# Kernel tuning notes

Measured on AMD Instinct MI355X. Metric: run time of the kernel, lower is better.

The kernel has to match this reference:

```python
import jax, jax.numpy as jnp
import numpy as np

N, K, R = 32768, 4096, 256

def setup_inputs() -> dict:
    key = jax.random.key(0)
    k1, k2, k3 = jax.random.split(key, 3)
    H = jax.random.normal(k1, (N, R), dtype=jnp.float32)
    L = jax.random.normal(k2, (K, R), dtype=jnp.float32)
    W_I = jax.random.normal(k3, (R, R), dtype=jnp.float32)
    return {"H": H, "L": L, "W_I": W_I}

def reference(H, L, W_I):
    # Q = W_I @ L^T : (r, k)
    Q = jnp.einsum('rs,ks->rk', W_I, L)
    # M_I = H @ Q : (n, k)
    M_I = jnp.einsum('nr,rk->nk', H, Q)
    A_I = jax.nn.softmax(M_I, axis=1)
    # C_I = A_I @ L : (n, r)
    C_I = jnp.einsum('nk,kr->nr', A_I, L)
    return (C_I, A_I)
```

## Files before the change

### kernel.cpp

```cpp
#include <hip/hip_runtime.h>
#include <hip/hip_bf16.h>
#include <math.h>
#include <stdint.h>

constexpr int N_ROWS = 32768;
constexpr int K_DIM  = 4096;
constexpr int R_DIM  = 256;
constexpr int KP     = 3 * R_DIM;
constexpr int KB     = K_DIM / 128;

typedef __bf16 bf16x8 __attribute__((ext_vector_type(8)));
typedef float  f32x4  __attribute__((ext_vector_type(4)));
typedef unsigned short u16x8 __attribute__((ext_vector_type(8)));
typedef unsigned short u16x4 __attribute__((ext_vector_type(4)));

__device__ __forceinline__ unsigned short f2bf(float x) {
    unsigned u = __float_as_uint(x);
    u += 0x7fffu + ((u >> 16) & 1u);
    return (unsigned short)(u >> 16);
}
__device__ __forceinline__ float bf2f(unsigned short h) {
    return __uint_as_float((unsigned)h << 16);
}

__device__ __forceinline__ void gl2lds16(const void* gptr, void* lptr) {
    __builtin_amdgcn_global_load_lds(
        (const __attribute__((address_space(1))) unsigned int*)gptr,
        (__attribute__((address_space(3))) unsigned int*)lptr,
        16, 0, 0);
}

__global__ __launch_bounds__(256)
void gemm_mfma_nt(const unsigned short* __restrict__ A,
                  const unsigned short* __restrict__ B,
                  float* __restrict__ C,
                  float* __restrict__ Pm, float* __restrict__ Ps,
                  int M, int N, int Kc)
{
    __shared__ __align__(16) unsigned short As[128 * 32];
    __shared__ __align__(16) unsigned short Bs[128 * 32];
    __shared__ float pm_s[128][2], ps_s[128][2];

    const int tid  = threadIdx.x;
    const int wave = tid >> 6, lane = tid & 63;
    const int wm = wave >> 1, wn = wave & 1;
    const long m0 = (long)blockIdx.x * 128;
    const long n0 = (long)blockIdx.y * 128;

    f32x4 acc[4][4] = {};

    const int srow  = lane >> 2;
    const int skoff = (lane & 3) * 8;
    const int c0 = wave, c1 = wave + 4;
    const int kq = (lane >> 4) * 8;
    const int mr = lane & 15;

    for (int k0 = 0; k0 < Kc; k0 += 32) {
        gl2lds16(A + (m0 + c0 * 16 + srow) * (long)Kc + k0 + skoff, &As[c0 * 512]);
        gl2lds16(A + (m0 + c1 * 16 + srow) * (long)Kc + k0 + skoff, &As[c1 * 512]);
        gl2lds16(B + (n0 + c0 * 16 + srow) * (long)Kc + k0 + skoff, &Bs[c0 * 512]);
        gl2lds16(B + (n0 + c1 * 16 + srow) * (long)Kc + k0 + skoff, &Bs[c1 * 512]);
        __syncthreads();

        bf16x8 af[4], bfr[4];
#pragma unroll
        for (int t = 0; t < 4; ++t) {
            af[t]  = *(const bf16x8*)&As[(wm * 64 + t * 16 + mr) * 32 + kq];
            bfr[t] = *(const bf16x8*)&Bs[(wn * 64 + t * 16 + mr) * 32 + kq];
        }
#pragma unroll
        for (int i = 0; i < 4; ++i)
#pragma unroll
            for (int j = 0; j < 4; ++j)
                acc[i][j] = __builtin_amdgcn_mfma_f32_16x16x32_bf16(
                    af[i], bfr[j], acc[i][j], 0, 0, 0);
        __syncthreads();
    }

    const int col = lane & 15, rquad = (lane >> 4) * 4;
#pragma unroll
    for (int i = 0; i < 4; ++i) {
        const long mrow = m0 + wm * 64 + i * 16 + rquad;
#pragma unroll
        for (int j = 0; j < 4; ++j) {
            float* p = C + mrow * (long)N + n0 + wn * 64 + j * 16 + col;
#pragma unroll
            for (int r = 0; r < 4; ++r) p[(long)r * N] = acc[i][j][r];
        }
    }

#pragma unroll
    for (int i = 0; i < 4; ++i) {
#pragma unroll
        for (int r = 0; r < 4; ++r) {
            float mx = fmaxf(fmaxf(acc[i][0][r], acc[i][1][r]),
                             fmaxf(acc[i][2][r], acc[i][3][r]));
#pragma unroll
            for (int off = 1; off < 16; off <<= 1)
                mx = fmaxf(mx, __shfl_xor(mx, off));
            float sm = 0.f;
#pragma unroll
            for (int j = 0; j < 4; ++j) sm += __expf(acc[i][j][r] - mx);
#pragma unroll
            for (int off = 1; off < 16; off <<= 1)
                sm += __shfl_xor(sm, off);
            if (mr == 0) {
                const int rw = wm * 64 + i * 16 + rquad + r;
                pm_s[rw][wn] = mx;
                ps_s[rw][wn] = sm;
            }
        }
    }
    __syncthreads();
    if (tid < 128) {
        const float ma = pm_s[tid][0], mb = pm_s[tid][1];
        const float mx = fmaxf(ma, mb);
        const float s  = ps_s[tid][0] * __expf(ma - mx) +
                         ps_s[tid][1] * __expf(mb - mx);
        Pm[(m0 + tid) * KB + blockIdx.y] = mx;
        Ps[(m0 + tid) * KB + blockIdx.y] = s;
    }
}

__global__ __launch_bounds__(256)
void finalize_ms(const float* __restrict__ Pm, const float* __restrict__ Ps,
                 float* __restrict__ SMm, float* __restrict__ SMi)
{
    const long row = (long)blockIdx.x * 256 + threadIdx.x;
    const float4* pm = (const float4*)(Pm + row * KB);
    const float4* ps = (const float4*)(Ps + row * KB);
    float4 v[8];
    float mx = -3.4e38f;
#pragma unroll
    for (int q = 0; q < 8; ++q) {
        v[q] = pm[q];
        mx = fmaxf(mx, fmaxf(fmaxf(v[q].x, v[q].y), fmaxf(v[q].z, v[q].w)));
    }
    float s = 0.f;
#pragma unroll
    for (int q = 0; q < 8; ++q) {
        float4 w = ps[q];
        s += w.x * __expf(v[q].x - mx) + w.y * __expf(v[q].y - mx) +
             w.z * __expf(v[q].z - mx) + w.w * __expf(v[q].w - mx);
    }
    SMm[row] = mx;
    SMi[row] = 1.f / s;
}

__global__ __launch_bounds__(512)
void softmax_av_pv(float* __restrict__ Mio,
                   const unsigned short* __restrict__ LT,
                   const float* __restrict__ SMm, const float* __restrict__ SMi,
                   float* __restrict__ C)
{
    __shared__ __align__(16) unsigned short Bs[R_DIM * 64];
    __shared__ __align__(16) unsigned short As[64 * 64];
    __shared__ float sm_m[64], sm_inv[64];

    const int tid  = threadIdx.x;
    const int wave = tid >> 6, lane = tid & 63;
    const long m0 = (long)blockIdx.x * 64;

    if (tid < 64) { sm_m[tid] = SMm[m0 + tid]; sm_inv[tid] = SMi[m0 + tid]; }
    __syncthreads();

    f32x4 acc[2][4] = {};
    const int wm = wave >> 2, wn = wave & 3;
    const int mr = lane & 15;
    const int kq16 = (lane >> 4) * 16;

    for (int k0 = 0; k0 < K_DIM; k0 += 64) {
#pragma unroll
        for (int q = 0; q < 4; ++q) {
            const int rbase = q * 64 + wave * 8;
            const int rloc  = rbase + (lane >> 3);
            const int phys  = (lane & 7) * 16;
            const int kbyte = phys ^ ((rloc & 7) << 4);
            gl2lds16((const char*)LT + (long)rloc * (K_DIM * 2) + (long)k0 * 2 + kbyte,
                     &Bs[rbase * 64]);
        }
#pragma unroll
        for (int p = 0; p < 2; ++p) {
            const int row = p * 32 + wave * 4 + (lane >> 4);
            const int col = (lane & 15) * 4;
            float* gp = Mio + (m0 + row) * (long)K_DIM + k0 + col;
            float4 v = *(const float4*)gp;
            const float mrow = sm_m[row], inv = sm_inv[row];
            float e0 = __expf(v.x - mrow), e1 = __expf(v.y - mrow);
            float e2 = __expf(v.z - mrow), e3 = __expf(v.w - mrow);
            *(float4*)gp = make_float4(e0 * inv, e1 * inv, e2 * inv, e3 * inv);
            u16x4 u;
            u[0] = f2bf(e0); u[1] = f2bf(e1); u[2] = f2bf(e2); u[3] = f2bf(e3);
            const int byte = (row * 128 + col * 2) ^ ((row & 7) << 4);
            *(u16x4*)((char*)As + byte) = u;
        }
        __syncthreads();

#pragma unroll
        for (int ks = 0; ks < 2; ++ks) {
            bf16x8 af[2], bfr[4];
#pragma unroll
            for (int t = 0; t < 2; ++t) {
                const int arow = wm * 32 + t * 16 + mr;
                const int ab = (arow * 128 + ks * 64 + kq16) ^ ((arow & 7) << 4);
                af[t] = *(const bf16x8*)((const char*)As + ab);
            }
#pragma unroll
            for (int t = 0; t < 4; ++t) {
                const int brow = wn * 64 + t * 16 + mr;
                const int bb = (brow * 128 + ks * 64 + kq16) ^ ((brow & 7) << 4);
                bfr[t] = *(const bf16x8*)((const char*)Bs + bb);
            }
#pragma unroll
            for (int i = 0; i < 2; ++i)
#pragma unroll
                for (int j = 0; j < 4; ++j)
                    acc[i][j] = __builtin_amdgcn_mfma_f32_16x16x32_bf16(
                        af[i], bfr[j], acc[i][j], 0, 0, 0);
        }
        __syncthreads();
    }

    const int col = lane & 15, rquad = (lane >> 4) * 4;
#pragma unroll
    for (int i = 0; i < 2; ++i) {
        const int lrow0 = wm * 32 + i * 16 + rquad;
#pragma unroll
        for (int j = 0; j < 4; ++j) {
            float* p = C + (m0 + lrow0) * (long)R_DIM + wn * 64 + j * 16 + col;
#pragma unroll
            for (int r = 0; r < 4; ++r)
                p[(long)r * R_DIM] = acc[i][j][r] * sm_inv[lrow0 + r];
        }
    }
}

__global__ __launch_bounds__(256)
void prep_B(const float* __restrict__ L, unsigned short* __restrict__ Bp)
{
    const long i = (long)blockIdx.x * 256 + threadIdx.x;
    const long k = i >> 8; const int r = (int)(i & 255);
    const float x = L[i];
    const unsigned short hi = f2bf(x);
    const unsigned short lo = f2bf(x - bf2f(hi));
    unsigned short* row = Bp + k * KP;
    row[r] = hi; row[R_DIM + r] = lo; row[2 * R_DIM + r] = hi;
}

__global__ __launch_bounds__(256)
void prep_LT(const float* __restrict__ L, unsigned short* __restrict__ LT)
{
    const long i = (long)blockIdx.x * 256 + threadIdx.x;
    const long r = i >> 12; const long k = i & 4095;
    LT[r * K_DIM + k] = f2bf(L[k * R_DIM + r]);
}

template<bool BT>
__global__ __launch_bounds__(256)
void gemm128(const float* __restrict__ A, const float* __restrict__ B,
             float* __restrict__ C, int M, int N, int Kc)
{
    __shared__ __align__(16) float Asl[16][132];
    __shared__ __align__(16) float Bsl[16][132];

    const int tid = threadIdx.x;
    const int tx = tid & 15, ty = tid >> 4;
    const long m0 = (long)blockIdx.x * 128;
    const long n0 = (long)blockIdx.y * 128;

    float acc[8][8];
#pragma unroll
    for (int i = 0; i < 8; ++i)
#pragma unroll
        for (int j = 0; j < 8; ++j) acc[i][j] = 0.f;

    for (int k0 = 0; k0 < Kc; k0 += 16) {
#pragma unroll
        for (int q = 0; q < 2; ++q) {
            int fi = tid + 256 * q, row = fi >> 2, col = (fi & 3) * 4;
            float4 v = *(const float4*)(A + (m0 + row) * (long)Kc + k0 + col);
            Asl[col + 0][row] = v.x; Asl[col + 1][row] = v.y;
            Asl[col + 2][row] = v.z; Asl[col + 3][row] = v.w;
        }
        if (BT) {
#pragma unroll
            for (int q = 0; q < 2; ++q) {
                int fi = tid + 256 * q, row = fi >> 2, col = (fi & 3) * 4;
                float4 v = *(const float4*)(B + (n0 + row) * (long)Kc + k0 + col);
                Bsl[col + 0][row] = v.x; Bsl[col + 1][row] = v.y;
                Bsl[col + 2][row] = v.z; Bsl[col + 3][row] = v.w;
            }
        } else {
#pragma unroll
            for (int q = 0; q < 2; ++q) {
                int fi = tid + 256 * q, row = fi >> 5, col = (fi & 31) * 4;
                float4 v = *(const float4*)(B + (k0 + row) * (long)N + n0 + col);
                *(float4*)&Bsl[row][col] = v;
            }
        }
        __syncthreads();
#pragma unroll
        for (int kk = 0; kk < 16; ++kk) {
            float a[8], b[8];
            *(float4*)&a[0] = *(const float4*)&Asl[kk][ty * 8];
            *(float4*)&a[4] = *(const float4*)&Asl[kk][ty * 8 + 4];
            *(float4*)&b[0] = *(const float4*)&Bsl[kk][tx * 8];
            *(float4*)&b[4] = *(const float4*)&Bsl[kk][tx * 8 + 4];
#pragma unroll
            for (int i = 0; i < 8; ++i)
#pragma unroll
                for (int j = 0; j < 8; ++j)
                    acc[i][j] = fmaf(a[i], b[j], acc[i][j]);
        }
        __syncthreads();
    }
#pragma unroll
    for (int i = 0; i < 8; ++i) {
        float* p = C + (m0 + ty * 8 + i) * (long)N + n0 + tx * 8;
        *(float4*)p       = make_float4(acc[i][0], acc[i][1], acc[i][2], acc[i][3]);
        *(float4*)(p + 4) = make_float4(acc[i][4], acc[i][5], acc[i][6], acc[i][7]);
    }
}

__global__ __launch_bounds__(256)
void gemm128_hl(const float* __restrict__ A, const float* __restrict__ B,
                unsigned short* __restrict__ Ap, int M, int N, int Kc)
{
    __shared__ __align__(16) float Asl[16][132];
    __shared__ __align__(16) float Bsl[16][132];

    const int tid = threadIdx.x;
    const int tx = tid & 15, ty = tid >> 4;
    const long m0 = (long)blockIdx.x * 128;
    const long n0 = (long)blockIdx.y * 128;

    float acc[8][8];
#pragma unroll
    for (int i = 0; i < 8; ++i)
#pragma unroll
        for (int j = 0; j < 8; ++j) acc[i][j] = 0.f;

    for (int k0 = 0; k0 < Kc; k0 += 16) {
#pragma unroll
        for (int q = 0; q < 2; ++q) {
            int fi = tid + 256 * q, row = fi >> 2, col = (fi & 3) * 4;
            float4 v = *(const float4*)(A + (m0 + row) * (long)Kc + k0 + col);
            Asl[col + 0][row] = v.x; Asl[col + 1][row] = v.y;
            Asl[col + 2][row] = v.z; Asl[col + 3][row] = v.w;
        }
#pragma unroll
        for (int q = 0; q < 2; ++q) {
            int fi = tid + 256 * q, row = fi >> 5, col = (fi & 31) * 4;
            float4 v = *(const float4*)(B + (k0 + row) * (long)N + n0 + col);
            *(float4*)&Bsl[row][col] = v;
        }
        __syncthreads();
#pragma unroll
        for (int kk = 0; kk < 16; ++kk) {
            float a[8], b[8];
            *(float4*)&a[0] = *(const float4*)&Asl[kk][ty * 8];
            *(float4*)&a[4] = *(const float4*)&Asl[kk][ty * 8 + 4];
            *(float4*)&b[0] = *(const float4*)&Bsl[kk][tx * 8];
            *(float4*)&b[4] = *(const float4*)&Bsl[kk][tx * 8 + 4];
#pragma unroll
            for (int i = 0; i < 8; ++i)
#pragma unroll
                for (int j = 0; j < 8; ++j)
                    acc[i][j] = fmaf(a[i], b[j], acc[i][j]);
        }
        __syncthreads();
    }
#pragma unroll
    for (int i = 0; i < 8; ++i) {
        const long row = m0 + ty * 8 + i;
        const int  cb  = (int)n0 + tx * 8;
        u16x8 vh, vl;
#pragma unroll
        for (int j = 0; j < 8; ++j) {
            const float x = acc[i][j];
            const unsigned short hi = f2bf(x);
            vh[j] = hi;
            vl[j] = f2bf(x - bf2f(hi));
        }
        unsigned short* rp = Ap + row * KP;
        *(u16x8*)(rp + cb)             = vh;
        *(u16x8*)(rp + R_DIM + cb)     = vh;
        *(u16x8*)(rp + 2 * R_DIM + cb) = vl;
    }
}

__global__ __launch_bounds__(256)
void softmax_rows(float* __restrict__ Mio)
{
    const long n  = blockIdx.x;
    float* row    = Mio + n * (long)K_DIM;
    const int tid = threadIdx.x;

    float4 v[4];
    float lmax = -3.4e38f;
#pragma unroll
    for (int q = 0; q < 4; ++q) {
        v[q] = ((const float4*)row)[tid + 256 * q];
        lmax = fmaxf(lmax, fmaxf(fmaxf(v[q].x, v[q].y), fmaxf(v[q].z, v[q].w)));
    }
    __shared__ float redmax[4], redsum[4];
#pragma unroll
    for (int off = 32; off > 0; off >>= 1)
        lmax = fmaxf(lmax, __shfl_xor(lmax, off));
    if ((tid & 63) == 0) redmax[tid >> 6] = lmax;
    __syncthreads();
    const float gmax = fmaxf(fmaxf(redmax[0], redmax[1]), fmaxf(redmax[2], redmax[3]));

    float lsum = 0.f;
#pragma unroll
    for (int q = 0; q < 4; ++q) {
        v[q].x = __expf(v[q].x - gmax); v[q].y = __expf(v[q].y - gmax);
        v[q].z = __expf(v[q].z - gmax); v[q].w = __expf(v[q].w - gmax);
        lsum += v[q].x + v[q].y + v[q].z + v[q].w;
    }
#pragma unroll
    for (int off = 32; off > 0; off >>= 1)
        lsum += __shfl_xor(lsum, off);
    if ((tid & 63) == 0) redsum[tid >> 6] = lsum;
    __syncthreads();
    const float inv = 1.f / (redsum[0] + redsum[1] + redsum[2] + redsum[3]);
#pragma unroll
    for (int q = 0; q < 4; ++q) {
        v[q].x *= inv; v[q].y *= inv; v[q].z *= inv; v[q].w *= inv;
        ((float4*)row)[tid + 256 * q] = v[q];
    }
}

extern "C" void kernel_launch(void* const* d_in, const int* in_sizes, int n_in,
                              void* d_out, int out_size, void* d_ws, size_t ws_size,
                              hipStream_t stream)
{
    const float* H  = (const float*)d_in[0];
    const float* L  = (const float*)d_in[1];
    const float* Wi = (const float*)d_in[2];

    float* Cout = (float*)d_out;
    float* Aout = (float*)d_out + (size_t)N_ROWS * R_DIM;

    const size_t szAp = (size_t)N_ROWS * KP * 2;
    const size_t szBp = (size_t)K_DIM * KP * 2;
    const size_t szLT = (size_t)R_DIM * K_DIM * 2;
    const size_t szPm = (size_t)N_ROWS * KB * 4;
    const size_t szPs = (size_t)N_ROWS * KB * 4;
    const size_t szSM = (size_t)N_ROWS * 4;

    if (ws_size >= szAp + szBp + szLT + szPm + szPs + 2 * szSM) {
        char* w = (char*)d_ws;
        unsigned short* Ap = (unsigned short*)w;                 w += szAp;
        unsigned short* Bp = (unsigned short*)w;                 w += szBp;
        unsigned short* LT = (unsigned short*)w;                 w += szLT;
        float* Pm  = (float*)w;                                  w += szPm;
        float* Ps  = (float*)w;                                  w += szPs;
        float* SMm = (float*)w;                                  w += szSM;
        float* SMi = (float*)w;

        gemm128_hl<<<dim3(N_ROWS / 128, R_DIM / 128), 256, 0, stream>>>(
            H, Wi, Ap, N_ROWS, R_DIM, R_DIM);
        prep_B<<<dim3((K_DIM * R_DIM) / 256), 256, 0, stream>>>(L, Bp);
        prep_LT<<<dim3((R_DIM * K_DIM) / 256), 256, 0, stream>>>(L, LT);
        gemm_mfma_nt<<<dim3(N_ROWS / 128, K_DIM / 128), 256, 0, stream>>>(
            Ap, Bp, Aout, Pm, Ps, N_ROWS, K_DIM, KP);
        finalize_ms<<<dim3(N_ROWS / 256), 256, 0, stream>>>(Pm, Ps, SMm, SMi);
        softmax_av_pv<<<dim3(N_ROWS / 64), 512, 0, stream>>>(
            Aout, LT, SMm, SMi, Cout);
    } else {
        gemm128<false><<<dim3(N_ROWS / 128, R_DIM / 128), 256, 0, stream>>>(
            H, Wi, Cout, N_ROWS, R_DIM, R_DIM);
        gemm128<true><<<dim3(N_ROWS / 128, K_DIM / 128), 256, 0, stream>>>(
            Cout, L, Aout, N_ROWS, K_DIM, R_DIM);
        softmax_rows<<<dim3(N_ROWS), 256, 0, stream>>>(Aout);
        gemm128<false><<<dim3(N_ROWS / 128, R_DIM / 128), 256, 0, stream>>>(
            Aout, L, Cout, N_ROWS, R_DIM, K_DIM);
    }
}
```

Baseline: 1.256 ms.

## Swizzle GEMM block order for L2 reuse and prefetch softmax inputs

The logits GEMM now uses a 1D grid with a grouped block mapping, so groups of 32 row-tiles sweep all column tiles together. This is meant to improve L2 reuse of the A and B operands. The softmax-AV kernel now loads the next M_I chunk into registers before the MFMA loop of the current chunk, hiding global-load latency behind compute. The cost is more live registers in the second kernel.

After: 1.205 ms. 1.04x faster.

```diff
diff --git a/kernel.cpp b/kernel.cpp
--- a/kernel.cpp
+++ b/kernel.cpp
@@ -44,8 +44,13 @@
     const int tid  = threadIdx.x;
     const int wave = tid >> 6, lane = tid & 63;
     const int wm = wave >> 1, wn = wave & 1;
-    const long m0 = (long)blockIdx.x * 128;
-    const long n0 = (long)blockIdx.y * 128;
+
+    const int bid = blockIdx.x;
+    const int xg = bid >> 10;
+    const int yb = (bid >> 5) & 31;
+    const int xi = bid & 31;
+    const long m0 = (long)(xg * 32 + xi) * 128;
+    const long n0 = (long)yb * 128;
 
     f32x4 acc[4][4] = {};
 
@@ -117,8 +122,8 @@
         const float mx = fmaxf(ma, mb);
         const float s  = ps_s[tid][0] * __expf(ma - mx) +
                          ps_s[tid][1] * __expf(mb - mx);
-        Pm[(m0 + tid) * KB + blockIdx.y] = mx;
-        Ps[(m0 + tid) * KB + blockIdx.y] = s;
+        Pm[(m0 + tid) * KB + yb] = mx;
+        Ps[(m0 + tid) * KB + yb] = s;
     }
 }
 
@@ -169,7 +174,21 @@
     const int mr = lane & 15;
     const int kq16 = (lane >> 4) * 16;
 
-    for (int k0 = 0; k0 < K_DIM; k0 += 64) {
+    const int arow0 = wave * 4 + (lane >> 4);
+    const int arow1 = 32 + arow0;
+    const int acolE = (lane & 15) * 4;
+    float* const gp0 = Mio + (m0 + arow0) * (long)K_DIM + acolE;
+    float* const gp1 = Mio + (m0 + arow1) * (long)K_DIM + acolE;
+    const int ab0 = (arow0 * 128 + acolE * 2) ^ ((arow0 & 7) << 4);
+    const int ab1 = (arow1 * 128 + acolE * 2) ^ ((arow1 & 7) << 4);
+    const float mm0 = sm_m[arow0], ii0 = sm_inv[arow0];
+    const float mm1 = sm_m[arow1], ii1 = sm_inv[arow1];
+
+    float4 va0 = *(const float4*)gp0;
+    float4 va1 = *(const float4*)gp1;
+
+    for (int t = 0; t < K_DIM / 64; ++t) {
+        const int k0 = t * 64;
 #pragma unroll
         for (int q = 0; q < 4; ++q) {
             const int rbase = q * 64 + wave * 8;
@@ -179,37 +198,40 @@
             gl2lds16((const char*)LT + (long)rloc * (K_DIM * 2) + (long)k0 * 2 + kbyte,
                      &Bs[rbase * 64]);
         }
-#pragma unroll
-        for (int p = 0; p < 2; ++p) {
-            const int row = p * 32 + wave * 4 + (lane >> 4);
-            const int col = (lane & 15) * 4;
-            float* gp = Mio + (m0 + row) * (long)K_DIM + k0 + col;
-            float4 v = *(const float4*)gp;
-            const float mrow = sm_m[row], inv = sm_inv[row];
-            float e0 = __expf(v.x - mrow), e1 = __expf(v.y - mrow);
-            float e2 = __expf(v.z - mrow), e3 = __expf(v.w - mrow);
-            *(float4*)gp = make_float4(e0 * inv, e1 * inv, e2 * inv, e3 * inv);
-            u16x4 u;
-            u[0] = f2bf(e0); u[1] = f2bf(e1); u[2] = f2bf(e2); u[3] = f2bf(e3);
-            const int byte = (row * 128 + col * 2) ^ ((row & 7) << 4);
-            *(u16x4*)((char*)As + byte) = u;
-        }
-        __syncthreads();
+        {
+            float e0 = __expf(va0.x - mm0), e1 = __expf(va0.y - mm0);
+            float e2 = __expf(va0.z - mm0), e3 = __expf(va0.w - mm0);
+            *(float4*)(gp0 + k0) = make_float4(e0 * ii0, e1 * ii0, e2 * ii0, e3 * ii0);
+            u16x4 u0; u0[0] = f2bf(e0); u0[1] = f2bf(e1); u0[2] = f2bf(e2); u0[3] = f2bf(e3);
+            *(u16x4*)((char*)As + ab0) = u0;
+
+            float f0 = __expf(va1.x - mm1), f1 = __expf(va1.y - mm1);
+            float f2 = __expf(va1.z - mm1), f3 = __expf(va1.w - mm1);
+            *(float4*)(gp1 + k0) = make_float4(f0 * ii1, f1 * ii1, f2 * ii1, f3 * ii1);
+            u16x4 u1; u1[0] = f2bf(f0); u1[1] = f2bf(f1); u1[2] = f2bf(f2); u1[3] = f2bf(f3);
+            *(u16x4*)((char*)As + ab1) = u1;
+        }
+        __syncthreads();
+
+        if (t + 1 < K_DIM / 64) {
+            va0 = *(const float4*)(gp0 + k0 + 64);
+            va1 = *(const float4*)(gp1 + k0 + 64);
+        }
 
 #pragma unroll
         for (int ks = 0; ks < 2; ++ks) {
             bf16x8 af[2], bfr[4];
 #pragma unroll
-            for (int t = 0; t < 2; ++t) {
-                const int arow = wm * 32 + t * 16 + mr;
+            for (int tt = 0; tt < 2; ++tt) {
+                const int arow = wm * 32 + tt * 16 + mr;
                 const int ab = (arow * 128 + ks * 64 + kq16) ^ ((arow & 7) << 4);
-                af[t] = *(const bf16x8*)((const char*)As + ab);
+                af[tt] = *(const bf16x8*)((const char*)As + ab);
             }
 #pragma unroll
-            for (int t = 0; t < 4; ++t) {
-                const int brow = wn * 64 + t * 16 + mr;
+            for (int tt = 0; tt < 4; ++tt) {
+                const int brow = wn * 64 + tt * 16 + mr;
                 const int bb = (brow * 128 + ks * 64 + kq16) ^ ((brow & 7) << 4);
-                bfr[t] = *(const bf16x8*)((const char*)Bs + bb);
+                bfr[tt] = *(const bf16x8*)((const char*)Bs + bb);
             }
 #pragma unroll
             for (int i = 0; i < 2; ++i)
@@ -463,7 +485,7 @@
             H, Wi, Ap, N_ROWS, R_DIM, R_DIM);
         prep_B<<<dim3((K_DIM * R_DIM) / 256), 256, 0, stream>>>(L, Bp);
         prep_LT<<<dim3((R_DIM * K_DIM) / 256), 256, 0, stream>>>(L, LT);
-        gemm_mfma_nt<<<dim3(N_ROWS / 128, K_DIM / 128), 256, 0, stream>>>(
+        gemm_mfma_nt<<<dim3((N_ROWS / 128) * (K_DIM / 128)), 256, 0, stream>>>(
             Ap, Bp, Aout, Pm, Ps, N_ROWS, K_DIM, KP);
         finalize_ms<<<dim3(N_ROWS / 256), 256, 0, stream>>>(Pm, Ps, SMm, SMi);
         softmax_av_pv<<<dim3(N_ROWS / 64), 512, 0, stream>>>(
```
